# Kernel tuning notes

Measured on AMD Instinct MI355X. Metric: run time of the kernel, lower is better.

The kernel has to match this reference:

```python
import jax, jax.numpy as jnp
import numpy as np
import math

N_HEAD = 12


def setup_inputs() -> dict:
    key = jax.random.key(0)
    ks = jax.random.split(key, 4)
    B, T, C = 8, 1024, 768
    s = 0.02
    return {
        "x": jax.random.normal(ks[0], (B, T, C), dtype=jnp.float32),
        "attn_mask": jnp.ones((B, T), dtype=jnp.int32),
        "W_attn": jax.random.normal(ks[1], (C, 3 * C), dtype=jnp.float32) * s,
        "b_attn": jnp.zeros((3 * C,), dtype=jnp.float32),
        "W_proj": jax.random.normal(ks[2], (C, C), dtype=jnp.float32) * s,
        "b_proj": jnp.zeros((C,), dtype=jnp.float32),
    }


def reference(x, attn_mask, W_attn, b_attn, W_proj, b_proj):
    B, T, C = x.shape
    hd = C // N_HEAD
    qkv = x @ W_attn + b_attn                      # [B, T, 3C]
    q, k, v = jnp.split(qkv, 3, axis=2)
    # [B, H, T, hd]
    q = q.reshape(B, T, N_HEAD, hd).transpose(0, 2, 1, 3)
    k = k.reshape(B, T, N_HEAD, hd).transpose(0, 2, 1, 3)
    v = v.reshape(B, T, N_HEAD, hd).transpose(0, 2, 1, 3)
    scores = jnp.einsum("bhqd,bhkd->bhqk", q, k) * (1.0 / math.sqrt(hd))
    mask = attn_mask[:, None, None, :]             # [B, 1, 1, T] broadcast over H, q
    scores = jnp.where(mask == 0, -jnp.inf, scores)
    attn = jax.nn.softmax(scores, axis=-1)
    out = jnp.einsum("bhqk,bhkd->bhqd", attn, v)   # [B, H, T, hd]
    out = out.transpose(0, 2, 1, 3).reshape(B, T, C)
    return out @ W_proj + b_proj
```

## Files before the change

kernel.cpp:

```cpp
#include <hip/hip_runtime.h>
#include <hip/hip_bf16.h>
#include <math.h>

constexpr int Bsz  = 8;
constexpr int Tseq = 1024;
constexpr int Cdim = 768;
constexpr int NH   = 12;
constexpr int HD   = 64;
constexpr int Mrows = Bsz * Tseq;
constexpr int C3    = 3 * Cdim;

using short8  = __attribute__((ext_vector_type(8))) short;
using s4v     = __attribute__((ext_vector_type(4))) short;
using floatx4 = __attribute__((ext_vector_type(4))) float;
using uintx4  = __attribute__((ext_vector_type(4))) unsigned int;

__device__ __forceinline__ unsigned short f32_to_bf16_rn(float f) {
    unsigned int u = __float_as_uint(f);
    unsigned int r = u + 0x7FFFu + ((u >> 16) & 1u);
    return (unsigned short)(r >> 16);
}
__device__ __forceinline__ unsigned pack_bf16x2_rn(float a, float b) {
    float2 f2; f2.x = a; f2.y = b;
    __hip_bfloat162 h = __float22bfloat162_rn(f2);
    unsigned r;
    __builtin_memcpy(&r, &h, sizeof(r));
    return r;
}
__device__ __forceinline__ short8 lds_ld8(const unsigned short* p) {
    s4v a = *(const s4v*)p;
    s4v b = *(const s4v*)(p + 4);
    return __builtin_shufflevector(a, b, 0, 1, 2, 3, 4, 5, 6, 7);
}
__device__ __forceinline__ void lds_st8(unsigned short* p, short8 v) {
    *(s4v*)p       = __builtin_shufflevector(v, v, 0, 1, 2, 3);
    *(s4v*)(p + 4) = __builtin_shufflevector(v, v, 4, 5, 6, 7);
}

#define GLOAD_LDS16(g, l) __builtin_amdgcn_global_load_lds(                    \
    (const __attribute__((address_space(1))) void*)(g),                        \
    (__attribute__((address_space(3))) void*)(l), 16, 0, 0)

#define WAITVM0 asm volatile("s_waitcnt vmcnt(0)" ::: "memory")

__global__ __launch_bounds__(256)
void to_bf16(const float* __restrict__ in, unsigned short* __restrict__ out, int n4)
{
    int t = blockIdx.x * blockDim.x + threadIdx.x;
    if (t >= n4) return;
    float4 v = ((const float4*)in)[t];
    ushort4 o;
    o.x = f32_to_bf16_rn(v.x);
    o.y = f32_to_bf16_rn(v.y);
    o.z = f32_to_bf16_rn(v.z);
    o.w = f32_to_bf16_rn(v.w);
    ((ushort4*)out)[t] = o;
}

__global__ __launch_bounds__(256)
void transpose_bf16(const float* __restrict__ in, unsigned short* __restrict__ out,
                    int K, int N)
{
    __shared__ float tile[32][33];
    const int k0 = blockIdx.y * 32, n0 = blockIdx.x * 32;
    const int tx = threadIdx.x & 31, ty = threadIdx.x >> 5;
    #pragma unroll
    for (int r = ty; r < 32; r += 8)
        tile[r][tx] = in[(size_t)(k0 + r) * N + n0 + tx];
    __syncthreads();
    #pragma unroll
    for (int r = ty; r < 32; r += 8)
        out[(size_t)(n0 + r) * K + k0 + tx] = f32_to_bf16_rn(tile[tx][r]);
}

template<int MH>
__device__ __forceinline__ void qkv_body(
    const unsigned short* __restrict__ A_g,
    const unsigned short* __restrict__ B_g,
    const float* __restrict__ bias,
    unsigned short* __restrict__ Cb,
    const int row0, const int col0, const int K, const int N,
    unsigned short* lds)
{
    constexpr int BK   = 32;
    constexpr int BUFS = 16384;

    const int tid  = threadIdx.x;
    const int wave = tid >> 6;
    const int lane = tid & 63;
    const int lm   = lane & 15;
    const int quad = lane >> 4;
    const int wy   = wave >> 2;
    const int wx   = wave & 3;
    const int NI   = K / BK;
    const int sq8  = (quad ^ ((lm ^ (lm >> 2)) & 3)) * 8;
    const int sr   = tid >> 2;
    const int sq   = tid & 3;

    floatx4 acc[4 * MH][4] = {};

    auto stageA = [&](int buf, int k0, int h) {
        const int r  = h * 128 + sr;
        const int gc = k0 + ((sq ^ ((r ^ (r >> 2)) & 3)) << 3);
        GLOAD_LDS16(A_g + (size_t)(row0 + r) * K + gc,
                    lds + buf * BUFS + r * 32 + sq * 8);
    };
    auto stageB = [&](int buf, int k0, int h) {
        const int r  = h * 128 + sr;
        const int gc = k0 + ((sq ^ ((r ^ (r >> 2)) & 3)) << 3);
        GLOAD_LDS16(B_g + (size_t)(col0 + r) * K + gc,
                    lds + buf * BUFS + 8192 + r * 32 + sq * 8);
    };

    #pragma unroll
    for (int h = 0; h < MH; ++h) stageA(0, 0, h);
    stageB(0, 0, 0); stageB(0, 0, 1);
    #pragma unroll
    for (int h = 0; h < MH; ++h) stageA(1, BK, h);
    stageB(1, BK, 0); stageB(1, BK, 1);
    if constexpr (MH == 2) asm volatile("s_waitcnt vmcnt(4)" ::: "memory");
    else                   asm volatile("s_waitcnt vmcnt(3)" ::: "memory");
    __builtin_amdgcn_s_barrier();

    short8 af[2 * MH], bf[4];
    int cur = 0;
    for (int kt = 0; kt < NI; ++kt) {
        const unsigned short* bufA = lds + cur * BUFS;
        const unsigned short* bufB = bufA + 8192;
        const int  stg  = (cur + 2 >= 3) ? cur - 1 : cur + 2;
        const int  k2   = (kt + 2) * BK;
        const bool doSt = (kt + 2 < NI);

        #pragma unroll
        for (int u = 0; u < 2 * MH; ++u)
            af[u] = *(const short8*)(bufA + (wy * (64 * MH) + u * 16 + lm) * 32 + sq8);
        #pragma unroll
        for (int j = 0; j < 4; ++j)
            bf[j] = *(const short8*)(bufB + (wx * 64 + j * 16 + lm) * 32 + sq8);
        if (doSt) {
            stageA(stg, k2, 0);
            if constexpr (MH == 2) stageA(stg, k2, 1); else stageB(stg, k2, 0);
        }
        __builtin_amdgcn_s_barrier();
        __builtin_amdgcn_s_setprio(1);
        #pragma unroll
        for (int u = 0; u < 2 * MH; ++u)
            #pragma unroll
            for (int j = 0; j < 4; ++j)
                acc[u][j] = __builtin_amdgcn_mfma_f32_16x16x32_bf16(af[u], bf[j], acc[u][j], 0, 0, 0);
        __builtin_amdgcn_s_setprio(0);
        __builtin_amdgcn_s_barrier();

        #pragma unroll
        for (int u = 0; u < 2 * MH; ++u)
            af[u] = *(const short8*)(bufA + (wy * (64 * MH) + (2 * MH + u) * 16 + lm) * 32 + sq8);
        if (doSt) {
            if constexpr (MH == 2) { stageB(stg, k2, 0); stageB(stg, k2, 1); }
            else                   stageB(stg, k2, 1);
        }
        __builtin_amdgcn_s_barrier();
        __builtin_amdgcn_s_setprio(1);
        #pragma unroll
        for (int u = 0; u < 2 * MH; ++u)
            #pragma unroll
            for (int j = 0; j < 4; ++j)
                acc[2 * MH + u][j] = __builtin_amdgcn_mfma_f32_16x16x32_bf16(af[u], bf[j], acc[2 * MH + u][j], 0, 0, 0);
        __builtin_amdgcn_s_setprio(0);
        if (kt == NI - 2) { WAITVM0; }
        else if (kt < NI - 2) {
            if constexpr (MH == 2) asm volatile("s_waitcnt vmcnt(4)" ::: "memory");
            else                   asm volatile("s_waitcnt vmcnt(3)" ::: "memory");
        }
        __builtin_amdgcn_s_barrier();

        cur = (cur == 2) ? 0 : cur + 1;
    }
    asm volatile("" ::: "memory");

    unsigned short* wbuf = lds + (NI % 3) * BUFS + wave * 1088;
    float bvj[4];
    #pragma unroll
    for (int j = 0; j < 4; ++j) bvj[j] = bias[col0 + wx * 64 + j * 16 + lm];
    #pragma unroll
    for (int i = 0; i < 4 * MH; ++i) {
        #pragma unroll
        for (int j = 0; j < 4; ++j) {
            #pragma unroll
            for (int r = 0; r < 4; ++r)
                wbuf[(quad * 4 + r) * 68 + j * 16 + lm] = f32_to_bf16_rn(acc[i][j][r] + bvj[j]);
        }
        asm volatile("s_waitcnt lgkmcnt(0)" ::: "memory");
        #pragma unroll
        for (int p = 0; p < 2; ++p) {
            const int lrow  = p * 8 + (lane >> 3);
            const int lcol8 = (lane & 7) * 8;
            short8 v = lds_ld8(&wbuf[lrow * 68 + lcol8]);
            *(short8*)(Cb + (size_t)(row0 + wy * (64 * MH) + i * 16 + lrow) * N +
                       col0 + wx * 64 + lcol8) = v;
        }
        asm volatile("s_waitcnt lgkmcnt(0)" ::: "memory");
    }
}

__global__ __launch_bounds__(512, 1)
void gemm_qkv8p(const unsigned short* __restrict__ A_g,
                const unsigned short* __restrict__ B_g,
                const float* __restrict__ bias,
                unsigned short* __restrict__ Cb)
{
    __shared__ __align__(16) unsigned short lds[3 * 16384];
    const int bid = blockIdx.x;
    if (bid < 256) {
        const int sid = (bid & 7) * 32 + (bid >> 3);
        qkv_body<2>(A_g, B_g, bias, Cb,
                    (sid >> 3) * 256, (sid & 7) * 256, Cdim, C3, lds);
    } else {
        const int t   = bid - 256;
        const int sid = (t & 7) * 8 + (t >> 3);
        qkv_body<1>(A_g, B_g, bias, Cb, sid * 128, 2048, Cdim, C3, lds);
    }
}

__global__ __launch_bounds__(256)
void gemm_proj(const unsigned short* __restrict__ AO_g,
               const unsigned short* __restrict__ B_g,
               const float* __restrict__ bias,
               float* __restrict__ C,
               int M, int N, int K)
{
    __shared__ __align__(16) unsigned short Ah[2][128 * 32];
    __shared__ __align__(16) unsigned short Bh[2][128 * 32];

    const int tid  = threadIdx.x;
    const int wave = tid >> 6;
    const int lane = tid & 63;
    const int lm   = lane & 15;
    const int quad = lane >> 4;
    const int wy   = wave >> 1, wx = wave & 1;
    const int row0 = blockIdx.y * 128;
    const int col0 = blockIdx.x * 128;

    const int sr  = lane >> 2;
    const int skp = (lane & 3) * 8;
    const int NI  = K / 32;

    floatx4 acc[4][4] = {};

    {
        const int head0 = skp >> 6, off0 = skp & 63;
        #pragma unroll
        for (int s = 0; s < 2; ++s) {
            const int r = (wave * 2 + s) * 16 + sr;
            GLOAD_LDS16(AO_g + (size_t)head0 * (Mrows * HD) + (size_t)(row0 + r) * HD + off0,
                        &Ah[0][r * 32 + skp]);
            GLOAD_LDS16(B_g + (size_t)(col0 + r) * K + skp, &Bh[0][r * 32 + skp]);
        }
    }
    __syncthreads();

    for (int kt = 0; kt < NI; ++kt) {
        const int cur = kt & 1, nxt = cur ^ 1;

        if (kt + 1 < NI) {
            const int k0   = (kt + 1) * 32;
            const int kk   = k0 + skp;
            const int head = kk >> 6;
            const int off  = kk & 63;
            #pragma unroll
            for (int s = 0; s < 2; ++s) {
                const int r = (wave * 2 + s) * 16 + sr;
                GLOAD_LDS16(AO_g + (size_t)head * (Mrows * HD) + (size_t)(row0 + r) * HD + off,
                            &Ah[nxt][r * 32 + skp]);
                GLOAD_LDS16(B_g + (size_t)(col0 + r) * K + k0 + skp, &Bh[nxt][r * 32 + skp]);
            }
        }

        short8 af[4];
        #pragma unroll
        for (int i = 0; i < 4; ++i)
            af[i] = *(const short8*)&Ah[cur][(wy * 64 + i * 16 + lm) * 32 + quad * 8];
        #pragma unroll
        for (int j = 0; j < 4; ++j) {
            short8 bfj = *(const short8*)&Bh[cur][(wx * 64 + j * 16 + lm) * 32 + quad * 8];
            #pragma unroll
            for (int i = 0; i < 4; ++i)
                acc[i][j] = __builtin_amdgcn_mfma_f32_16x16x32_bf16(af[i], bfj, acc[i][j], 0, 0, 0);
        }

        __syncthreads();
    }

    #pragma unroll
    for (int j = 0; j < 4; ++j) {
        const int col = col0 + wx * 64 + j * 16 + lm;
        const float bv = bias[col];
        #pragma unroll
        for (int i = 0; i < 4; ++i) {
            const int rowb = row0 + wy * 64 + i * 16 + quad * 4;
            #pragma unroll
            for (int r = 0; r < 4; ++r)
                C[(size_t)(rowb + r) * N + col] = acc[i][j][r] + bv;
        }
    }
}

__global__ __launch_bounds__(256, 3)
void attn_bf16(const unsigned short* __restrict__ qkv,
               const int* __restrict__ mask,
               unsigned short* __restrict__ outh)
{
    constexpr int LDW = 68;
    constexpr int NT  = Tseq / 64;
    __shared__ __align__(16) unsigned short Kh[2][64 * LDW];
    __shared__ __align__(16) unsigned short Vh[2][64 * LDW];
    __shared__ float maskadd[2][64];
    __shared__ int   mflag[2];

    const int tid  = threadIdx.x;
    const int wave = tid >> 6;
    const int lane = tid & 63;
    const int lm   = lane & 15;
    const int quad = lane >> 4;
    const int idx  = blockIdx.x;
    const int bh   = idx % (Bsz * NH);
    const int qb   = idx / (Bsz * NH);
    const int b    = bh / NH;
    const int h    = bh % NH;
    const int q0   = qb * 128;
    const float scale = 0.125f;

    short8 qf[2][2];
    #pragma unroll
    for (int mt = 0; mt < 2; ++mt) {
        const size_t qrow = (size_t)(b * Tseq + q0 + wave * 32 + mt * 16 + lm) * C3 + h * HD;
        #pragma unroll
        for (int kf = 0; kf < 2; ++kf)
            qf[mt][kf] = *(const short8*)(qkv + qrow + kf * 32 + quad * 8);
    }

    const int tr0 = (tid & 31) * 2;
    const int sc  = (tid >> 5) * 8;
    const int ps0 = (tr0 & 0x27) | ((tr0 & 0x10) >> 1) | ((tr0 & 0x08) << 1);
    const int smi = (tid & 0x27) | ((tid & 0x10) >> 1) | ((tid & 0x08) << 1);

    short8 kh0, kh1, vh0, vh1;
    float  mreg = 0.f;

    {
        const size_t g0 = (size_t)(b * Tseq + tr0) * C3 + Cdim + h * HD + sc;
        kh0 = *(const short8*)(qkv + g0);
        kh1 = *(const short8*)(qkv + g0 + C3);
        vh0 = *(const short8*)(qkv + g0 + Cdim);
        vh1 = *(const short8*)(qkv + g0 + Cdim + C3);
        lds_st8(&Kh[0][ps0 * LDW + sc], kh0);
        lds_st8(&Kh[0][(ps0 + 1) * LDW + sc], kh1);
        #pragma unroll
        for (int i = 0; i < 8; ++i) {
            unsigned int pv = (unsigned int)(unsigned short)vh0[i] |
                              ((unsigned int)(unsigned short)vh1[i] << 16);
            *(unsigned int*)&Vh[0][(sc + i) * LDW + tr0] = pv;
        }
        if (tid < 64) {
            mreg = (mask[b * Tseq + tid] == 0) ? -1e30f : 0.0f;
            const int f = __all(mreg == 0.0f);
            maskadd[0][smi] = mreg;
            if (tid == 0) mflag[0] = f;
        }
    }
    __syncthreads();

    floatx4 O[2][4] = {};
    float lsum[2] = {0.f, 0.f};

    for (int kt = 0; kt < NT; ++kt) {
        const int cur = kt & 1;
        const int nxt = cur ^ 1;
        const unsigned short* Khc = Kh[cur];
        const unsigned short* Vhc = Vh[cur];

        if (kt + 1 < NT) {
            const size_t g0 = (size_t)(b * Tseq + (kt + 1) * 64 + tr0) * C3 + Cdim + h * HD + sc;
            kh0 = *(const short8*)(qkv + g0);
            kh1 = *(const short8*)(qkv + g0 + C3);
            vh0 = *(const short8*)(qkv + g0 + Cdim);
            vh1 = *(const short8*)(qkv + g0 + Cdim + C3);
            if (tid < 64) mreg = (mask[b * Tseq + (kt + 1) * 64 + tid] == 0) ? -1e30f : 0.0f;
        }

        floatx4 S[2][4] = {};
        #pragma unroll
        for (int kf = 0; kf < 2; ++kf) {
            short8 kh[4];
            #pragma unroll
            for (int nt = 0; nt < 4; ++nt)
                kh[nt] = lds_ld8(&Khc[(nt * 16 + lm) * LDW + kf * 32 + quad * 8]);
            #pragma unroll
            for (int mt = 0; mt < 2; ++mt)
                #pragma unroll
                for (int nt = 0; nt < 4; ++nt)
                    S[mt][nt] = __builtin_amdgcn_mfma_f32_16x16x32_bf16(kh[nt], qf[mt][kf], S[mt][nt], 0, 0, 0);
        }

        const int nomask = mflag[cur];

        unsigned X[2][8];
        if (nomask) {
            #pragma unroll
            for (int mt = 0; mt < 2; ++mt) {
                #pragma unroll
                for (int nt = 0; nt < 4; ++nt) {
                    float p0 = __expf(S[mt][nt][0] * scale);
                    float p1 = __expf(S[mt][nt][1] * scale);
                    float p2 = __expf(S[mt][nt][2] * scale);
                    float p3 = __expf(S[mt][nt][3] * scale);
                    lsum[mt] += p0; lsum[mt] += p1;
                    lsum[mt] += p2; lsum[mt] += p3;
                    X[mt][nt * 2 + 0] = pack_bf16x2_rn(p0, p1);
                    X[mt][nt * 2 + 1] = pack_bf16x2_rn(p2, p3);
                }
            }
        } else {
            float madd[4][4];
            #pragma unroll
            for (int nt = 0; nt < 4; ++nt)
                #pragma unroll
                for (int r = 0; r < 4; ++r)
                    madd[nt][r] = maskadd[cur][nt * 16 + quad * 4 + r];
            #pragma unroll
            for (int mt = 0; mt < 2; ++mt) {
                #pragma unroll
                for (int nt = 0; nt < 4; ++nt) {
                    float p0 = __expf(S[mt][nt][0] * scale + madd[nt][0]);
                    float p1 = __expf(S[mt][nt][1] * scale + madd[nt][1]);
                    float p2 = __expf(S[mt][nt][2] * scale + madd[nt][2]);
                    float p3 = __expf(S[mt][nt][3] * scale + madd[nt][3]);
                    lsum[mt] += p0; lsum[mt] += p1;
                    lsum[mt] += p2; lsum[mt] += p3;
                    X[mt][nt * 2 + 0] = pack_bf16x2_rn(p0, p1);
                    X[mt][nt * 2 + 1] = pack_bf16x2_rn(p2, p3);
                }
            }
        }

        const bool qodd = (quad & 1);
        short8 pf[2][2];
        #pragma unroll
        for (int mt = 0; mt < 2; ++mt) {
            #pragma unroll
            for (int pr = 0; pr < 4; ++pr) {
                const int a  = (pr & 1) | ((pr & 2) << 1);
                const int b2 = a + 2;
                unsigned t = qodd ? X[mt][a] : X[mt][b2];
                t = (unsigned)__shfl_xor((int)t, 16);
                X[mt][a]  = qodd ? t : X[mt][a];
                X[mt][b2] = qodd ? X[mt][b2] : t;
            }
            uintx4 u0 = {X[mt][0], X[mt][1], X[mt][2], X[mt][3]};
            uintx4 u1 = {X[mt][4], X[mt][5], X[mt][6], X[mt][7]};
            __builtin_memcpy(&pf[mt][0], &u0, 16);
            __builtin_memcpy(&pf[mt][1], &u1, 16);
        }

        #pragma unroll
        for (int kf = 0; kf < 2; ++kf) {
            #pragma unroll
            for (int dt = 0; dt < 4; ++dt) {
                short8 vh = lds_ld8(&Vhc[(dt * 16 + lm) * LDW + kf * 32 + quad * 8]);
                #pragma unroll
                for (int mt = 0; mt < 2; ++mt)
                    O[mt][dt] = __builtin_amdgcn_mfma_f32_16x16x32_bf16(vh, pf[mt][kf], O[mt][dt], 0, 0, 0);
            }
        }

        if (kt + 1 < NT) {
            lds_st8(&Kh[nxt][ps0 * LDW + sc], kh0);
            lds_st8(&Kh[nxt][(ps0 + 1) * LDW + sc], kh1);
            #pragma unroll
            for (int i = 0; i < 8; ++i) {
                unsigned int pv = (unsigned int)(unsigned short)vh0[i] |
                                  ((unsigned int)(unsigned short)vh1[i] << 16);
                *(unsigned int*)&Vh[nxt][(sc + i) * LDW + tr0] = pv;
            }
            if (tid < 64) {
                const int f = __all(mreg == 0.0f);
                maskadd[nxt][smi] = mreg;
                if (tid == 0) mflag[nxt] = f;
            }
        }
        __syncthreads();
    }

    #pragma unroll
    for (int mt = 0; mt < 2; ++mt) {
        lsum[mt] += __shfl_xor(lsum[mt], 16);
        lsum[mt] += __shfl_xor(lsum[mt], 32);
        const float inv_l = 1.0f / lsum[mt];
        const size_t row = (size_t)h * (Mrows * HD) +
                           (size_t)(b * Tseq + q0 + wave * 32 + mt * 16 + lm) * HD;
        #pragma unroll
        for (int dt = 0; dt < 4; ++dt) {
            ushort4 hv;
            unsigned short* hp = &hv.x;
            #pragma unroll
            for (int r = 0; r < 4; ++r)
                hp[r] = f32_to_bf16_rn(O[mt][dt][r] * inv_l);
            *(ushort4*)(outh + row + dt * 16 + quad * 4) = hv;
        }
    }
}

extern "C" void kernel_launch(void* const* d_in, const int* in_sizes, int n_in,
                              void* d_out, int out_size, void* d_ws, size_t ws_size,
                              hipStream_t stream)
{
    const float* x      = (const float*)d_in[0];
    const int*   mask   = (const int*)  d_in[1];
    const float* W_attn = (const float*)d_in[2];
    const float* b_attn = (const float*)d_in[3];
    const float* W_proj = (const float*)d_in[4];
    const float* b_proj = (const float*)d_in[5];
    float* out = (float*)d_out;

    unsigned short* xh    = (unsigned short*)d_ws;
    unsigned short* wat_h = xh    + (size_t)Mrows * Cdim;
    unsigned short* wpt_h = wat_h + (size_t)C3 * Cdim;
    unsigned short* qkvh  = wpt_h + (size_t)Cdim * Cdim;
    unsigned short* aoh   = xh;

    dim3 blk(256);

    to_bf16<<<dim3(Mrows * Cdim / 4 / 256), blk, 0, stream>>>(x, xh, Mrows * Cdim / 4);
    transpose_bf16<<<dim3(C3 / 32, Cdim / 32), blk, 0, stream>>>(W_attn, wat_h, Cdim, C3);
    transpose_bf16<<<dim3(Cdim / 32, Cdim / 32), blk, 0, stream>>>(W_proj, wpt_h, Cdim, Cdim);

    gemm_qkv8p<<<dim3(320), dim3(512), 0, stream>>>(xh, wat_h, b_attn, qkvh);

    attn_bf16<<<dim3((Tseq / 128) * Bsz * NH), blk, 0, stream>>>(qkvh, mask, aoh);

    gemm_proj<<<dim3(Cdim / 128, Mrows / 128), blk, 0, stream>>>(
        aoh, wpt_h, b_proj, out, Mrows, Cdim, Cdim);
}
```

Baseline: 208.2 us.

## Unify QKV and projection GEMMs into one 128x256 triple-buffered tile body

Replaces the 512-thread mixed-tile QKV GEMM and the simple double-buffered projection GEMM with one templated 128x256 kernel body. It uses 256 threads, swizzled LDS and 3-stage async global-to-LDS staging, and targets two blocks per CU. The projection GEMM now gets the pipelined, swizzled path with a grouped block order. The QKV GEMM gets a uniform 576-block grid instead of 320 blocks of mixed shape. Each wave now holds a 128x64 accumulator slice, which raises register pressure, and the projection launches only 192 blocks, which may underfill the CUs.

```diff
diff --git a/kernel.cpp b/kernel.cpp
--- a/kernel.cpp
+++ b/kernel.cpp
@@ -73,103 +73,104 @@
         out[(size_t)(n0 + r) * K + k0 + tx] = f32_to_bf16_rn(tile[tx][r]);
 }
 
-template<int MH>
-__device__ __forceinline__ void qkv_body(
+template<bool HM, bool B16>
+__device__ __forceinline__ void gemm_body_128x256(
     const unsigned short* __restrict__ A_g,
     const unsigned short* __restrict__ B_g,
     const float* __restrict__ bias,
-    unsigned short* __restrict__ Cb,
+    void* __restrict__ Cout,
     const int row0, const int col0, const int K, const int N,
     unsigned short* lds)
 {
     constexpr int BK   = 32;
-    constexpr int BUFS = 16384;
+    constexpr int ABUF = 4096;
+    constexpr int BUFS = 12288;
 
     const int tid  = threadIdx.x;
     const int wave = tid >> 6;
     const int lane = tid & 63;
     const int lm   = lane & 15;
     const int quad = lane >> 4;
-    const int wy   = wave >> 2;
-    const int wx   = wave & 3;
     const int NI   = K / BK;
     const int sq8  = (quad ^ ((lm ^ (lm >> 2)) & 3)) * 8;
     const int sr   = tid >> 2;
     const int sq   = tid & 3;
 
-    floatx4 acc[4 * MH][4] = {};
-
-    auto stageA = [&](int buf, int k0, int h) {
-        const int r  = h * 128 + sr;
-        const int gc = k0 + ((sq ^ ((r ^ (r >> 2)) & 3)) << 3);
-        GLOAD_LDS16(A_g + (size_t)(row0 + r) * K + gc,
-                    lds + buf * BUFS + r * 32 + sq * 8);
+    floatx4 acc[8][4] = {};
+
+    auto stageA = [&](int buf, int k0) {
+        #pragma unroll
+        for (int s = 0; s < 2; ++s) {
+            const int r  = s * 64 + sr;
+            const int gc = ((sq ^ ((r ^ (r >> 2)) & 3)) << 3);
+            if constexpr (HM) {
+                const int head = k0 >> 6;
+                const int off  = (k0 & 63) + gc;
+                GLOAD_LDS16(A_g + (size_t)head * (Mrows * HD) +
+                            (size_t)(row0 + r) * HD + off,
+                            lds + buf * BUFS + r * 32 + sq * 8);
+            } else {
+                GLOAD_LDS16(A_g + (size_t)(row0 + r) * K + k0 + gc,
+                            lds + buf * BUFS + r * 32 + sq * 8);
+            }
+        }
     };
-    auto stageB = [&](int buf, int k0, int h) {
-        const int r  = h * 128 + sr;
-        const int gc = k0 + ((sq ^ ((r ^ (r >> 2)) & 3)) << 3);
-        GLOAD_LDS16(B_g + (size_t)(col0 + r) * K + gc,
-                    lds + buf * BUFS + 8192 + r * 32 + sq * 8);
+    auto stageB = [&](int buf, int k0) {
+        #pragma unroll
+        for (int s = 0; s < 4; ++s) {
+            const int r  = s * 64 + sr;
+            const int gc = ((sq ^ ((r ^ (r >> 2)) & 3)) << 3);
+            GLOAD_LDS16(B_g + (size_t)(col0 + r) * K + k0 + gc,
+                        lds + buf * BUFS + ABUF + r * 32 + sq * 8);
+        }
     };
 
-    #pragma unroll
-    for (int h = 0; h < MH; ++h) stageA(0, 0, h);
-    stageB(0, 0, 0); stageB(0, 0, 1);
-    #pragma unroll
-    for (int h = 0; h < MH; ++h) stageA(1, BK, h);
-    stageB(1, BK, 0); stageB(1, BK, 1);
-    if constexpr (MH == 2) asm volatile("s_waitcnt vmcnt(4)" ::: "memory");
-    else                   asm volatile("s_waitcnt vmcnt(3)" ::: "memory");
+    stageA(0, 0);  stageB(0, 0);
+    stageA(1, BK); stageB(1, BK);
+    asm volatile("s_waitcnt vmcnt(6)" ::: "memory");
     __builtin_amdgcn_s_barrier();
 
-    short8 af[2 * MH], bf[4];
+    short8 af[4], bf[4];
     int cur = 0;
     for (int kt = 0; kt < NI; ++kt) {
         const unsigned short* bufA = lds + cur * BUFS;
-        const unsigned short* bufB = bufA + 8192;
+        const unsigned short* bufB = bufA + ABUF;
         const int  stg  = (cur + 2 >= 3) ? cur - 1 : cur + 2;
         const int  k2   = (kt + 2) * BK;
         const bool doSt = (kt + 2 < NI);
 
         #pragma unroll
-        for (int u = 0; u < 2 * MH; ++u)
-            af[u] = *(const short8*)(bufA + (wy * (64 * MH) + u * 16 + lm) * 32 + sq8);
+        for (int i = 0; i < 4; ++i)
+            af[i] = *(const short8*)(bufA + (i * 16 + lm) * 32 + sq8);
         #pragma unroll
         for (int j = 0; j < 4; ++j)
-            bf[j] = *(const short8*)(bufB + (wx * 64 + j * 16 + lm) * 32 + sq8);
-        if (doSt) {
-            stageA(stg, k2, 0);
-            if constexpr (MH == 2) stageA(stg, k2, 1); else stageB(stg, k2, 0);
-        }
+            bf[j] = *(const short8*)(bufB + (wave * 64 + j * 16 + lm) * 32 + sq8);
+        if (doSt) stageA(stg, k2);
         __builtin_amdgcn_s_barrier();
         __builtin_amdgcn_s_setprio(1);
         #pragma unroll
-        for (int u = 0; u < 2 * MH; ++u)
+        for (int i = 0; i < 4; ++i)
             #pragma unroll
             for (int j = 0; j < 4; ++j)
-                acc[u][j] = __builtin_amdgcn_mfma_f32_16x16x32_bf16(af[u], bf[j], acc[u][j], 0, 0, 0);
+                acc[i][j] = __builtin_amdgcn_mfma_f32_16x16x32_bf16(af[i], bf[j], acc[i][j], 0, 0, 0);
         __builtin_amdgcn_s_setprio(0);
         __builtin_amdgcn_s_barrier();
 
         #pragma unroll
-        for (int u = 0; u < 2 * MH; ++u)
-            af[u] = *(const short8*)(bufA + (wy * (64 * MH) + (2 * MH + u) * 16 + lm) * 32 + sq8);
-        if (doSt) {
-            if constexpr (MH == 2) { stageB(stg, k2, 0); stageB(stg, k2, 1); }
-            else                   stageB(stg, k2, 1);
-        }
+        for (int i = 0; i < 4; ++i)
+            af[i] = *(const short8*)(bufA + ((4 + i) * 16 + lm) * 32 + sq8);
+        if (doSt) stageB(stg, k2);
         __builtin_amdgcn_s_barrier();
         __builtin_amdgcn_s_setprio(1);
         #pragma unroll
-        for (int u = 0; u < 2 * MH; ++u)
+        for (int i = 0; i < 4; ++i)
             #pragma unroll
             for (int j = 0; j < 4; ++j)
-                acc[2 * MH + u][j] = __builtin_amdgcn_mfma_f32_16x16x32_bf16(af[u], bf[j], acc[2 * MH + u][j], 0, 0, 0);
+                acc[4 + i][j] = __builtin_amdgcn_mfma_f32_16x16x32_bf16(af[i], bf[j], acc[4 + i][j], 0, 0, 0);
         __builtin_amdgcn_s_setprio(0);
         if (kt == NI - 2) { WAITVM0; }
         else if (kt < NI - 2) {
-            if constexpr (MH == 2) asm volatile("s_waitcnt vmcnt(4)" ::: "memory");
-            else                   asm volatile("s_waitcnt vmcnt(3)" ::: "memory");
+            asm volatile("s_waitcnt vmcnt(6)" ::: "memory");
         }
         __builtin_amdgcn_s_barrier();
 
@@ -177,131 +178,76 @@
     }
     asm volatile("" ::: "memory");
 
-    unsigned short* wbuf = lds + (NI % 3) * BUFS + wave * 1088;
-    float bvj[4];
-    #pragma unroll
-    for (int j = 0; j < 4; ++j) bvj[j] = bias[col0 + wx * 64 + j * 16 + lm];
-    #pragma unroll
-    for (int i = 0; i < 4 * MH; ++i) {
+    if constexpr (B16) {
+        unsigned short* Cb   = (unsigned short*)Cout;
+        unsigned short* wbuf = lds + (NI % 3) * BUFS + wave * 1088;
+        float bvj[4];
+        #pragma unroll
+        for (int j = 0; j < 4; ++j) bvj[j] = bias[col0 + wave * 64 + j * 16 + lm];
+        #pragma unroll
+        for (int i = 0; i < 8; ++i) {
+            #pragma unroll
+            for (int j = 0; j < 4; ++j) {
+                #pragma unroll
+                for (int r = 0; r < 4; ++r)
+                    wbuf[(quad * 4 + r) * 68 + j * 16 + lm] = f32_to_bf16_rn(acc[i][j][r] + bvj[j]);
+            }
+            asm volatile("s_waitcnt lgkmcnt(0)" ::: "memory");
+            #pragma unroll
+            for (int p = 0; p < 2; ++p) {
+                const int lrow  = p * 8 + (lane >> 3);
+                const int lcol8 = (lane & 7) * 8;
+                short8 v = lds_ld8(&wbuf[lrow * 68 + lcol8]);
+                *(short8*)(Cb + (size_t)(row0 + i * 16 + lrow) * N +
+                           col0 + wave * 64 + lcol8) = v;
+            }
+            asm volatile("s_waitcnt lgkmcnt(0)" ::: "memory");
+        }
+    } else {
+        float* C = (float*)Cout;
         #pragma unroll
         for (int j = 0; j < 4; ++j) {
-            #pragma unroll
-            for (int r = 0; r < 4; ++r)
-                wbuf[(quad * 4 + r) * 68 + j * 16 + lm] = f32_to_bf16_rn(acc[i][j][r] + bvj[j]);
-        }
-        asm volatile("s_waitcnt lgkmcnt(0)" ::: "memory");
-        #pragma unroll
-        for (int p = 0; p < 2; ++p) {
-            const int lrow  = p * 8 + (lane >> 3);
-            const int lcol8 = (lane & 7) * 8;
-            short8 v = lds_ld8(&wbuf[lrow * 68 + lcol8]);
-            *(short8*)(Cb + (size_t)(row0 + wy * (64 * MH) + i * 16 + lrow) * N +
-                       col0 + wx * 64 + lcol8) = v;
-        }
-        asm volatile("s_waitcnt lgkmcnt(0)" ::: "memory");
-    }
-}
-
-__global__ __launch_bounds__(512, 1)
-void gemm_qkv8p(const unsigned short* __restrict__ A_g,
-                const unsigned short* __restrict__ B_g,
-                const float* __restrict__ bias,
-                unsigned short* __restrict__ Cb)
-{
-    __shared__ __align__(16) unsigned short lds[3 * 16384];
+            const int col = col0 + wave * 64 + j * 16 + lm;
+            const float bv = bias[col];
+            #pragma unroll
+            for (int i = 0; i < 8; ++i) {
+                const int rowb = row0 + i * 16 + quad * 4;
+                #pragma unroll
+                for (int r = 0; r < 4; ++r)
+                    C[(size_t)(rowb + r) * N + col] = acc[i][j][r] + bv;
+            }
+        }
+    }
+}
+
+__global__ __launch_bounds__(256, 2)
+void gemm_qkv128(const unsigned short* __restrict__ A_g,
+                 const unsigned short* __restrict__ B_g,
+                 const float* __restrict__ bias,
+                 unsigned short* __restrict__ Cb)
+{
+    __shared__ __align__(16) unsigned short lds[3 * 12288];
     const int bid = blockIdx.x;
-    if (bid < 256) {
-        const int sid = (bid & 7) * 32 + (bid >> 3);
-        qkv_body<2>(A_g, B_g, bias, Cb,
-                    (sid >> 3) * 256, (sid & 7) * 256, Cdim, C3, lds);
-    } else {
-        const int t   = bid - 256;
-        const int sid = (t & 7) * 8 + (t >> 3);
-        qkv_body<1>(A_g, B_g, bias, Cb, sid * 128, 2048, Cdim, C3, lds);
-    }
-}
-
-__global__ __launch_bounds__(256)
-void gemm_proj(const unsigned short* __restrict__ AO_g,
-               const unsigned short* __restrict__ B_g,
-               const float* __restrict__ bias,
-               float* __restrict__ C,
-               int M, int N, int K)
-{
-    __shared__ __align__(16) unsigned short Ah[2][128 * 32];
-    __shared__ __align__(16) unsigned short Bh[2][128 * 32];
-
-    const int tid  = threadIdx.x;
-    const int wave = tid >> 6;
-    const int lane = tid & 63;
-    const int lm   = lane & 15;
-    const int quad = lane >> 4;
-    const int wy   = wave >> 1, wx = wave & 1;
-    const int row0 = blockIdx.y * 128;
-    const int col0 = blockIdx.x * 128;
-
-    const int sr  = lane >> 2;
-    const int skp = (lane & 3) * 8;
-    const int NI  = K / 32;
-
-    floatx4 acc[4][4] = {};
-
-    {
-        const int head0 = skp >> 6, off0 = skp & 63;
-        #pragma unroll
-        for (int s = 0; s < 2; ++s) {
-            const int r = (wave * 2 + s) * 16 + sr;
-            GLOAD_LDS16(AO_g + (size_t)head0 * (Mrows * HD) + (size_t)(row0 + r) * HD + off0,
-                        &Ah[0][r * 32 + skp]);
-            GLOAD_LDS16(B_g + (size_t)(col0 + r) * K + skp, &Bh[0][r * 32 + skp]);
-        }
-    }
-    __syncthreads();
-
-    for (int kt = 0; kt < NI; ++kt) {
-        const int cur = kt & 1, nxt = cur ^ 1;
-
-        if (kt + 1 < NI) {
-            const int k0   = (kt + 1) * 32;
-            const int kk   = k0 + skp;
-            const int head = kk >> 6;
-            const int off  = kk & 63;
-            #pragma unroll
-            for (int s = 0; s < 2; ++s) {
-                const int r = (wave * 2 + s) * 16 + sr;
-                GLOAD_LDS16(AO_g + (size_t)head * (Mrows * HD) + (size_t)(row0 + r) * HD + off,
-                            &Ah[nxt][r * 32 + skp]);
-                GLOAD_LDS16(B_g + (size_t)(col0 + r) * K + k0 + skp, &Bh[nxt][r * 32 + skp]);
-            }
-        }
-
-        short8 af[4];
-        #pragma unroll
-        for (int i = 0; i < 4; ++i)
-            af[i] = *(const short8*)&Ah[cur][(wy * 64 + i * 16 + lm) * 32 + quad * 8];
-        #pragma unroll
-        for (int j = 0; j < 4; ++j) {
-            short8 bfj = *(const short8*)&Bh[cur][(wx * 64 + j * 16 + lm) * 32 + quad * 8];
-            #pragma unroll
-            for (int i = 0; i < 4; ++i)
-                acc[i][j] = __builtin_amdgcn_mfma_f32_16x16x32_bf16(af[i], bfj, acc[i][j], 0, 0, 0);
-        }
-
-        __syncthreads();
-    }
-
-    #pragma unroll
-    for (int j = 0; j < 4; ++j) {
-        const int col = col0 + wx * 64 + j * 16 + lm;
-        const float bv = bias[col];
-        #pragma unroll
-        for (int i = 0; i < 4; ++i) {
-            const int rowb = row0 + wy * 64 + i * 16 + quad * 4;
-            #pragma unroll
-            for (int r = 0; r < 4; ++r)
-                C[(size_t)(rowb + r) * N + col] = acc[i][j][r] + bv;
-        }
-    }
+    const int sid = (bid & 7) * 72 + (bid >> 3);
+    const int by  = sid & 63;
+    const int bx  = sid >> 6;
+    gemm_body_128x256<false, true>(A_g, B_g, bias, Cb,
+                                   by * 128, bx * 256, Cdim, C3, lds);
+}
+
+__global__ __launch_bounds__(256, 2)
+void gemm_proj128(const unsigned short* __restrict__ AO_g,
+                  const unsigned short* __restrict__ B_g,
+                  const float* __restrict__ bias,
+                  float* __restrict__ C)
+{
+    __shared__ __align__(16) unsigned short lds[3 * 12288];
+    const int bid = blockIdx.x;
+    const int sid = (bid & 7) * 24 + (bid >> 3);
+    const int by  = sid & 63;
+    const int bx  = sid >> 6;
+    gemm_body_128x256<true, false>(AO_g, B_g, bias, C,
+                                   by * 128, bx * 256, Cdim, Cdim, lds);
 }
 
 __global__ __launch_bounds__(256, 3)
@@ -533,10 +479,9 @@
     transpose_bf16<<<dim3(C3 / 32, Cdim / 32), blk, 0, stream>>>(W_attn, wat_h, Cdim, C3);
     transpose_bf16<<<dim3(Cdim / 32, Cdim / 32), blk, 0, stream>>>(W_proj, wpt_h, Cdim, Cdim);
 
-    gemm_qkv8p<<<dim3(320), dim3(512), 0, stream>>>(xh, wat_h, b_attn, qkvh);
+    gemm_qkv128<<<dim3(576), blk, 0, stream>>>(xh, wat_h, b_attn, qkvh);
 
     attn_bf16<<<dim3((Tseq / 128) * Bsz * NH), blk, 0, stream>>>(qkvh, mask, aoh);
 
-    gemm_proj<<<dim3(Cdim / 128, Mrows / 128), blk, 0, stream>>>(
-        aoh, wpt_h, b_proj, out, Mrows, Cdim, Cdim);
-}
+    gemm_proj128<<<dim3(192), blk, 0, stream>>>(aoh, wpt_h, b_proj, out);
+}
```

Measured after the change: 204.7 us. Within noise of the previous version (-1.7%).
